# Optimization experiments

Hardware: AMD Instinct MI355X
Metric: run time of the kernel (lower is better)

Reference implementation:

```python
import jax, jax.numpy as jnp
import numpy as np

ROUTING_ITERATIONS = 3

def squash(x, axis=-1):
    # norm_sq/(1+norm_sq) * x/norm, equation 1 of the CapsNet paper
    norm_sq = jnp.sum(x * x, axis=axis, keepdims=True)
    norm = jnp.sqrt(norm_sq)
    return norm_sq / (1.0 + norm_sq) * (x / norm)

def setup_inputs() -> dict:
    key = jax.random.key(0)
    k1, k2 = jax.random.split(key)
    B, IC, IH, OC, OH = 64, 2048, 16, 64, 32
    input_capsules = jax.random.normal(k1, (B, IC, IH), dtype=jnp.float32)
    # scale weight so U entries are O(1) (sum over in_hid=16)
    W = jax.random.normal(k2, (IC, IH, OC, OH), dtype=jnp.float32) * (1.0 / np.sqrt(IH))
    return {"input_capsules": input_capsules, "W": W}

def reference(input_capsules, W):
    # U[b,i,o,j] = sum_h x[b,i,h] * W[i,h,o,j]
    U = jnp.einsum('bih,ihoj->bioj', input_capsules, W)
    b, in_caps, out_caps, out_hid = U.shape
    Blog = jnp.zeros((b, in_caps, out_caps), dtype=U.dtype)

    def body(Blog, _):
        C = jax.nn.softmax(Blog, axis=-1)            # [b,i,o]
        S = jnp.einsum('bio,bioh->boh', C, U)        # [b,o,h]
        V = squash(S, axis=-1)                       # [b,o,h]
        Blog = Blog + jnp.einsum('bioh,boh->bio', U, V)
        return Blog, V

    _, Vs = jax.lax.scan(body, Blog, None, length=ROUTING_ITERATIONS)
    return Vs[-1]
```

## Files before the change

kernel.cpp:

```cpp
#include <hip/hip_runtime.h>
#include <hip/hip_bf16.h>
#include <cstdint>
#include <cstddef>

constexpr int B_SZ = 64, IC = 2048, IH = 16, OC = 64, OH = 32;
constexpr int NN = OC * OH;
constexpr int ICHUNK = 32;
constexpr int NCHUNK = IC / ICHUNK;
constexpr int BTILE = 16;

typedef __attribute__((ext_vector_type(8))) short bf16x8;
typedef __attribute__((ext_vector_type(4))) float f32x4;

constexpr int F_Z = 0;
constexpr int F_W = 64;
constexpr int F_WBUF = 65536;
constexpr int F_T = F_W + 2 * F_WBUF;
constexpr int T_ROW = 80;
constexpr int T_BUF = 16 * T_ROW;
constexpr int F_SMEM = F_T + 2 * T_BUF;

__device__ __forceinline__ unsigned short f2bf(float f) {
    unsigned u = __float_as_uint(f);
    u += 0x7fffu + ((u >> 16) & 1u);
    return (unsigned short)(u >> 16);
}
__device__ __forceinline__ float bf_lo(unsigned u) {
    return __uint_as_float(u << 16);
}
__device__ __forceinline__ float bf_hi(unsigned u) {
    return __uint_as_float(u & 0xffff0000u);
}
__device__ __forceinline__ unsigned pk2f(float a, float b) {
    return (unsigned)f2bf(a) | ((unsigned)f2bf(b) << 16);
}
__device__ __forceinline__ void gload_lds16(const void* g, void* l) {
    __builtin_amdgcn_global_load_lds(
        (const __attribute__((address_space(1))) void*)g,
        (__attribute__((address_space(3))) void*)l, 16, 0, 0);
}

__global__ void prep_wx(const float* __restrict__ W, unsigned short* __restrict__ Wp,
                        const float* __restrict__ x, unsigned short* __restrict__ xs) {
    int i = blockIdx.x;
    int t = threadIdx.x;
    const float* wp = W + (size_t)i * (IH * NN);
    int n0 = t * 4;
    float4 row[16];
#pragma unroll
    for (int h = 0; h < 16; ++h) row[h] = *(const float4*)(wp + h * NN + n0);
    char* dst = (char*)Wp + (size_t)i * 65536;
#pragma unroll
    for (int q = 0; q < 4; ++q) {
        float v[16];
#pragma unroll
        for (int h = 0; h < 16; ++h) v[h] = ((const float*)&row[h])[q];
        uint4 lo, hi;
        lo.x = pk2f(v[0], v[1]);   lo.y = pk2f(v[2], v[3]);
        lo.z = pk2f(v[4], v[5]);   lo.w = pk2f(v[6], v[7]);
        hi.x = pk2f(v[8], v[9]);   hi.y = pk2f(v[10], v[11]);
        hi.z = pk2f(v[12], v[13]); hi.w = pk2f(v[14], v[15]);
        *(uint4*)(dst + (size_t)(n0 + q) * 16) = lo;
        *(uint4*)(dst + 32768 + (size_t)(n0 + q) * 16) = hi;
    }
    if (t < 64) {
        const float* p = x + ((size_t)t * IC + i) * IH;
        unsigned short out[16];
#pragma unroll
        for (int h = 0; h < 16; ++h) out[h] = f2bf(p[h]);
        unsigned short* q = xs + ((size_t)i * 64 + t) * 16;
        *(uint4*)q = *(uint4*)&out[0];
        *(uint4*)(q + 8) = *(uint4*)&out[8];
    }
}

template <bool UNIFORM>
__launch_bounds__(1024, 4)
__global__ void routed_fast(const unsigned short* __restrict__ xs,
                            const unsigned short* __restrict__ Wp,
                            const float* __restrict__ Vin,
                            float* __restrict__ P) {
    extern __shared__ char smem[];
    const int tid = threadIdx.x;
    const int lane = tid & 63;
    const int wv = tid >> 6;
    const int l15 = lane & 15;
    const int g = lane >> 4;

    const int v = blockIdx.x;
    const int bt = (v >> 3) & 3;
    const int chunk = (v & 7) + 8 * (v >> 5);
    const int b0 = bt * BTILE;
    const int i0 = chunk * ICHUNK;

    if (tid < 16) ((unsigned*)(smem + F_Z))[tid] = 0u;

    uint4 vrp[4];
    if constexpr (!UNIFORM) {
#pragma unroll
        for (int o8 = 0; o8 < 4; ++o8) {
            const float* vb =
                Vin + ((size_t)(b0 + l15) * OC + (wv * 4 + o8)) * OH + g * 4;
            f32x4 a = *(const f32x4*)vb;
            f32x4 c = *(const f32x4*)(vb + 16);
            vrp[o8].x = pk2f(a.x, a.y);
            vrp[o8].y = pk2f(a.z, a.w);
            vrp[o8].z = pk2f(c.x, c.y);
            vrp[o8].w = pk2f(c.z, c.w);
        }
    }

    {
        const char* gs = (const char*)Wp + (size_t)i0 * 65536;
#pragma unroll
        for (int r = 0; r < 4; ++r) {
            int seg = r * 16 + wv;
            gload_lds16(gs + seg * 1024 + lane * 16, smem + F_W + seg * 1024);
        }
    }
    bf16x8 xf = {0, 0, 0, 0, 0, 0, 0, 0};
    if (lane < 32)
        xf = *(const bf16x8*)(xs + (size_t)i0 * 1024 + (size_t)(b0 + l15) * 16 + g * 8);
    asm volatile("s_waitcnt vmcnt(0) lgkmcnt(0)" ::: "memory");
    __builtin_amdgcn_s_barrier();

    const f32x4 fzero = {0.f, 0.f, 0.f, 0.f};
    f32x4 sacc[8];
#pragma unroll
    for (int t = 0; t < 8; ++t) sacc[t] = fzero;

    for (int ii = 0; ii < ICHUNK; ++ii) {
        const int cur = ii & 1;
        const char* wb = smem + F_W + cur * F_WBUF;
        const int i = i0 + ii;

        bf16x8 xf_n = {0, 0, 0, 0, 0, 0, 0, 0};
        if (ii + 1 < ICHUNK) {
            const char* gs = (const char*)Wp + (size_t)(i + 1) * 65536;
            char* lb = smem + F_W + (cur ^ 1) * F_WBUF;
#pragma unroll
            for (int r = 0; r < 4; ++r) {
                int seg = r * 16 + wv;
                gload_lds16(gs + seg * 1024 + lane * 16, lb + seg * 1024);
            }
            if (lane < 32)
                xf_n = *(const bf16x8*)(xs + (size_t)(i + 1) * 1024 +
                                        (size_t)(b0 + l15) * 16 + g * 8);
        }

        f32x4 acc[8];
#pragma unroll
        for (int t = 0; t < 8; ++t) {
            int nt = wv * 128 + (t >> 1) * 32 + (t & 1) * 16;
            const char* aptr = (lane < 32)
                ? (wb + g * 32768 + (size_t)(nt + l15) * 16)
                : (smem + F_Z);
            bf16x8 af = *(const bf16x8*)aptr;
            if constexpr (UNIFORM) {
                sacc[t] = __builtin_amdgcn_mfma_f32_16x16x32_bf16(af, xf, sacc[t], 0, 0, 0);
            } else {
                acc[t] = __builtin_amdgcn_mfma_f32_16x16x32_bf16(af, xf, fzero, 0, 0, 0);
            }
        }

        if constexpr (UNIFORM) {
            asm volatile("s_waitcnt vmcnt(0)" ::: "memory");
            __builtin_amdgcn_s_barrier();
        } else {
            float eb[4], s4;
#pragma unroll
            for (int o8 = 0; o8 < 4; ++o8) {
                f32x4 a0 = acc[2 * o8], a1 = acc[2 * o8 + 1];
                uint4 u = vrp[o8];
                float p = a0.x * bf_lo(u.x) + a0.y * bf_hi(u.x) +
                          a0.z * bf_lo(u.y) + a0.w * bf_hi(u.y) +
                          a1.x * bf_lo(u.z) + a1.y * bf_hi(u.z) +
                          a1.z * bf_lo(u.w) + a1.w * bf_hi(u.w);
                p += __shfl_xor(p, 16);
                p += __shfl_xor(p, 32);
                eb[o8] = __expf(p);
            }
            s4 = (eb[0] + eb[1]) + (eb[2] + eb[3]);

            if (lane < 16)
                *(float*)(smem + F_T + cur * T_BUF + l15 * T_ROW + wv * 4) = s4;

            asm volatile("s_waitcnt vmcnt(0) lgkmcnt(0)" ::: "memory");
            __builtin_amdgcn_s_barrier();

            const char* tb = smem + F_T + cur * T_BUF + l15 * T_ROW;
            f32x4 t0 = *(const f32x4*)(tb);
            f32x4 t1 = *(const f32x4*)(tb + 16);
            f32x4 t2 = *(const f32x4*)(tb + 32);
            f32x4 t3 = *(const f32x4*)(tb + 48);
            f32x4 ts = (t0 + t1) + (t2 + t3);
            float denom = (ts.x + ts.y) + (ts.z + ts.w);
            float rd = __builtin_amdgcn_rcpf(denom);
            float c0 = eb[0] * rd, c1 = eb[1] * rd, c2 = eb[2] * rd, c3 = eb[3] * rd;
#pragma unroll
            for (int t = 0; t < 8; ++t) {
                float c = (t < 2) ? c0 : (t < 4) ? c1 : (t < 6) ? c2 : c3;
                sacc[t] += acc[t] * c;
            }
        }
        xf = xf_n;
    }

    const float scale = UNIFORM ? (1.0f / 64.0f) : 1.0f;
#pragma unroll
    for (int t = 0; t < 8; ++t) {
        int n = wv * 128 + (t >> 1) * 32 + (t & 1) * 16 + g * 4;
        float* dst = P + ((size_t)(chunk * 64) + b0 + l15) * NN + n;
        float4 o4;
        o4.x = sacc[t].x * scale; o4.y = sacc[t].y * scale;
        o4.z = sacc[t].z * scale; o4.w = sacc[t].w * scale;
        *(float4*)dst = o4;
    }
}

__global__ void reduce_squash(const float* __restrict__ P, float* __restrict__ dst,
                              int addmode) {
    int pr = blockIdx.x * 2 + (threadIdx.x >> 5);
    int j = threadIdx.x & 31;
    int b = pr >> 6, o = pr & 63;
    const float* p = P + (size_t)b * NN + o * 32 + j;
    float s = 0.f;
#pragma unroll 8
    for (int c = 0; c < NCHUNK; ++c) s += p[(size_t)c * (64 * NN)];
    float nsq = s * s;
#pragma unroll
    for (int d = 16; d >= 1; d >>= 1) nsq += __shfl_xor(nsq, d);
    float nrm = sqrtf(nsq);
    float f = nrm / (1.f + nsq);
    float outv = s * f;
    int idx = pr * 32 + j;
    if (addmode) dst[idx] += outv;
    else dst[idx] = outv;
}

extern "C" void kernel_launch(void* const* d_in, const int* in_sizes, int n_in,
                              void* d_out, int out_size, void* d_ws, size_t ws_size,
                              hipStream_t stream) {
    const float* x = (const float*)d_in[0];
    const float* W = (const float*)d_in[1];
    float* out = (float*)d_out;
    char* ws = (char*)d_ws;
    unsigned short* xs = (unsigned short*)ws;
    float* P = (float*)(ws + ((size_t)4 << 20));
    float* Vsum = (float*)(ws + ((size_t)36 << 20));
    unsigned short* Wp = (unsigned short*)(ws + (((size_t)40) << 20));

    (void)hipFuncSetAttribute(reinterpret_cast<const void*>(&routed_fast<true>),
                              hipFuncAttributeMaxDynamicSharedMemorySize, F_SMEM);
    (void)hipFuncSetAttribute(reinterpret_cast<const void*>(&routed_fast<false>),
                              hipFuncAttributeMaxDynamicSharedMemorySize, F_SMEM);

    prep_wx<<<dim3(2048), dim3(512), 0, stream>>>(W, Wp, x, xs);
    routed_fast<true><<<dim3(256), dim3(1024), F_SMEM, stream>>>(xs, Wp, nullptr, P);
    reduce_squash<<<dim3(2048), dim3(64), 0, stream>>>(P, Vsum, 0);
    routed_fast<false><<<dim3(256), dim3(1024), F_SMEM, stream>>>(xs, Wp, Vsum, P);
    reduce_squash<<<dim3(2048), dim3(64), 0, stream>>>(P, Vsum, 1);
    routed_fast<false><<<dim3(256), dim3(1024), F_SMEM, stream>>>(xs, Wp, Vsum, P);
    reduce_squash<<<dim3(2048), dim3(64), 0, stream>>>(P, out, 0);
}
```

Before: 323.0 us.

## Split uniform pass into dedicated 32x32 MFMA GEMM kernel and streamline routed loop

Replaces the templated uniform-routing path with a separate kernel. It uses 512-thread blocks, splits each chunk's N dimension into quarters, tiles 32 batches per block and runs 32x32x16 bf16 MFMAs with a 32KB double-buffered static LDS tile. This should improve MFMA utilisation and occupancy for the first iteration, which needs no softmax. The routed kernel gains hoisted pointer and offset arithmetic, an unrolled two-buffer loop and a larger zero region so all 64 lanes load x directly. It also uses __syncthreads in place of explicit waitcnt plus barrier. The cost is more blocks and separate code paths to maintain.

```diff
diff --git a/kernel.cpp b/kernel.cpp
--- a/kernel.cpp
+++ b/kernel.cpp
@@ -3,7 +3,7 @@
 #include <cstdint>
 #include <cstddef>
 
-constexpr int B_SZ = 64, IC = 2048, IH = 16, OC = 64, OH = 32;
+constexpr int IC = 2048, IH = 16, OC = 64, OH = 32;
 constexpr int NN = OC * OH;
 constexpr int ICHUNK = 32;
 constexpr int NCHUNK = IC / ICHUNK;
@@ -11,9 +11,10 @@
 
 typedef __attribute__((ext_vector_type(8))) short bf16x8;
 typedef __attribute__((ext_vector_type(4))) float f32x4;
+typedef __attribute__((ext_vector_type(16))) float f32x16;
 
 constexpr int F_Z = 0;
-constexpr int F_W = 64;
+constexpr int F_W = 2048;
 constexpr int F_WBUF = 65536;
 constexpr int F_T = F_W + 2 * F_WBUF;
 constexpr int T_ROW = 80;
@@ -74,9 +75,88 @@
     }
 }
 
-template <bool UNIFORM>
+__launch_bounds__(512, 4)
+__global__ void uniform_gemm(const unsigned short* __restrict__ xs,
+                             const unsigned short* __restrict__ Wp,
+                             float* __restrict__ P) {
+    __shared__ char smem[32768];
+    const int tid = threadIdx.x;
+    const int lane = tid & 63;
+    const int wv = tid >> 6;
+    const int l31 = lane & 31;
+    const int hi = lane >> 5;
+
+    const int v = blockIdx.x;
+    const int chunk = (v & 7) + 8 * (v >> 6);
+    const int sub = (v >> 3) & 7;
+    const int b0 = (sub >> 2) * 32;
+    const int nq = sub & 3;
+    const int i0 = chunk * ICHUNK;
+    const int n0 = nq * 512;
+
+    const char* gW = (const char*)Wp + (size_t)i0 * 65536;
+    int goff[2], loff[2];
+#pragma unroll
+    for (int r = 0; r < 2; ++r) {
+        int m = wv * 2 + r, s = m >> 3, q = m & 7;
+        goff[r] = s * 32768 + n0 * 16 + q * 1024 + lane * 16;
+        loff[r] = s * 8192 + q * 1024;
+    }
+    const int abase = hi * 8192 + wv * 1024 + l31 * 16;
+    const char* gx = (const char*)xs + (size_t)i0 * 2048 + (b0 + l31) * 32 + hi * 16;
+
+#pragma unroll
+    for (int r = 0; r < 2; ++r) gload_lds16(gW + goff[r], smem + loff[r]);
+    bf16x8 xf = *(const bf16x8*)gx;
+    __syncthreads();
+
+    f32x16 sacc[2];
+#pragma unroll
+    for (int t = 0; t < 2; ++t)
+#pragma unroll
+        for (int k = 0; k < 16; ++k) sacc[t][k] = 0.f;
+
+    for (int pp = 0; pp < ICHUNK / 2; ++pp) {
+#pragma unroll
+        for (int cb = 0; cb < 2; ++cb) {
+            const int ii = pp * 2 + cb;
+            bf16x8 xf_n = xf;
+            if (ii + 1 < ICHUNK) {
+                const char* gWn = gW + (size_t)(ii + 1) * 65536;
+                char* nb = smem + (cb ^ 1) * 16384;
+#pragma unroll
+                for (int r = 0; r < 2; ++r) gload_lds16(gWn + goff[r], nb + loff[r]);
+                xf_n = *(const bf16x8*)(gx + (size_t)(ii + 1) * 2048);
+            }
+            const char* ab = smem + cb * 16384 + abase;
+#pragma unroll
+            for (int t = 0; t < 2; ++t) {
+                bf16x8 af = *(const bf16x8*)(ab + t * 512);
+                sacc[t] = __builtin_amdgcn_mfma_f32_32x32x16_bf16(af, xf, sacc[t], 0, 0, 0);
+            }
+            __syncthreads();
+            xf = xf_n;
+        }
+    }
+
+    float* Pb = P + ((size_t)(chunk * 64) + b0 + l31) * NN + n0;
+#pragma unroll
+    for (int t = 0; t < 2; ++t) {
+        int ntl = (wv * 2 + t) * 32;
+#pragma unroll
+        for (int q = 0; q < 4; ++q) {
+            float4 o4;
+            o4.x = sacc[t][4 * q + 0] * (1.0f / 64.0f);
+            o4.y = sacc[t][4 * q + 1] * (1.0f / 64.0f);
+            o4.z = sacc[t][4 * q + 2] * (1.0f / 64.0f);
+            o4.w = sacc[t][4 * q + 3] * (1.0f / 64.0f);
+            *(float4*)(Pb + ntl + 8 * q + 4 * hi) = o4;
+        }
+    }
+}
+
 __launch_bounds__(1024, 4)
-__global__ void routed_fast(const unsigned short* __restrict__ xs,
+__global__ void routed_soft(const unsigned short* __restrict__ xs,
                             const unsigned short* __restrict__ Wp,
                             const float* __restrict__ Vin,
                             float* __restrict__ P) {
@@ -93,81 +173,69 @@
     const int b0 = bt * BTILE;
     const int i0 = chunk * ICHUNK;
 
-    if (tid < 16) ((unsigned*)(smem + F_Z))[tid] = 0u;
+    if (tid < 512) ((unsigned*)(smem + F_Z))[tid] = 0u;
 
     uint4 vrp[4];
-    if constexpr (!UNIFORM) {
-#pragma unroll
-        for (int o8 = 0; o8 < 4; ++o8) {
-            const float* vb =
-                Vin + ((size_t)(b0 + l15) * OC + (wv * 4 + o8)) * OH + g * 4;
-            f32x4 a = *(const f32x4*)vb;
-            f32x4 c = *(const f32x4*)(vb + 16);
-            vrp[o8].x = pk2f(a.x, a.y);
-            vrp[o8].y = pk2f(a.z, a.w);
-            vrp[o8].z = pk2f(c.x, c.y);
-            vrp[o8].w = pk2f(c.z, c.w);
-        }
-    }
-
-    {
-        const char* gs = (const char*)Wp + (size_t)i0 * 65536;
-#pragma unroll
-        for (int r = 0; r < 4; ++r) {
-            int seg = r * 16 + wv;
-            gload_lds16(gs + seg * 1024 + lane * 16, smem + F_W + seg * 1024);
-        }
-    }
-    bf16x8 xf = {0, 0, 0, 0, 0, 0, 0, 0};
-    if (lane < 32)
-        xf = *(const bf16x8*)(xs + (size_t)i0 * 1024 + (size_t)(b0 + l15) * 16 + g * 8);
-    asm volatile("s_waitcnt vmcnt(0) lgkmcnt(0)" ::: "memory");
-    __builtin_amdgcn_s_barrier();
+#pragma unroll
+    for (int o8 = 0; o8 < 4; ++o8) {
+        const float* vb = Vin + ((size_t)(b0 + l15) * OC + (wv * 4 + o8)) * OH + g * 4;
+        f32x4 a = *(const f32x4*)vb;
+        f32x4 c = *(const f32x4*)(vb + 16);
+        vrp[o8].x = pk2f(a.x, a.y); vrp[o8].y = pk2f(a.z, a.w);
+        vrp[o8].z = pk2f(c.x, c.y); vrp[o8].w = pk2f(c.z, c.w);
+    }
+
+    const int a_off = g * 32768 + wv * 2048 + l15 * 16;
+    const char* a_p0 = (lane < 32) ? (smem + F_W + a_off) : (smem + F_Z);
+    const char* a_p1 = (lane < 32) ? (smem + F_W + F_WBUF + a_off) : (smem + F_Z);
+
+    const char* gW = (const char*)Wp + (size_t)i0 * 65536;
+    int goff[4], lds_off[4];
+#pragma unroll
+    for (int r = 0; r < 4; ++r) {
+        int seg = r * 16 + wv;
+        goff[r] = seg * 1024 + lane * 16;
+        lds_off[r] = F_W + seg * 1024;
+    }
+
+    const char* gx = (const char*)xs + (size_t)i0 * 2048 + (b0 + l15) * 32 + (g & 1) * 16;
+
+    char* t_w = smem + F_T + l15 * T_ROW + wv * 4;
+    const char* t_r = smem + F_T + l15 * T_ROW;
+
+#pragma unroll
+    for (int r = 0; r < 4; ++r) gload_lds16(gW + goff[r], smem + lds_off[r]);
+    bf16x8 xf = *(const bf16x8*)gx;
+    __syncthreads();
 
     const f32x4 fzero = {0.f, 0.f, 0.f, 0.f};
     f32x4 sacc[8];
 #pragma unroll
     for (int t = 0; t < 8; ++t) sacc[t] = fzero;
 
-    for (int ii = 0; ii < ICHUNK; ++ii) {
-        const int cur = ii & 1;
-        const char* wb = smem + F_W + cur * F_WBUF;
-        const int i = i0 + ii;
-
-        bf16x8 xf_n = {0, 0, 0, 0, 0, 0, 0, 0};
-        if (ii + 1 < ICHUNK) {
-            const char* gs = (const char*)Wp + (size_t)(i + 1) * 65536;
-            char* lb = smem + F_W + (cur ^ 1) * F_WBUF;
-#pragma unroll
-            for (int r = 0; r < 4; ++r) {
-                int seg = r * 16 + wv;
-                gload_lds16(gs + seg * 1024 + lane * 16, lb + seg * 1024);
-            }
-            if (lane < 32)
-                xf_n = *(const bf16x8*)(xs + (size_t)(i + 1) * 1024 +
-                                        (size_t)(b0 + l15) * 16 + g * 8);
-        }
-
-        f32x4 acc[8];
-#pragma unroll
-        for (int t = 0; t < 8; ++t) {
-            int nt = wv * 128 + (t >> 1) * 32 + (t & 1) * 16;
-            const char* aptr = (lane < 32)
-                ? (wb + g * 32768 + (size_t)(nt + l15) * 16)
-                : (smem + F_Z);
-            bf16x8 af = *(const bf16x8*)aptr;
-            if constexpr (UNIFORM) {
-                sacc[t] = __builtin_amdgcn_mfma_f32_16x16x32_bf16(af, xf, sacc[t], 0, 0, 0);
-            } else {
+    for (int pp = 0; pp < ICHUNK / 2; ++pp) {
+#pragma unroll
+        for (int cb = 0; cb < 2; ++cb) {
+            const int ii = pp * 2 + cb;
+
+            bf16x8 xf_n = xf;
+            if (ii + 1 < ICHUNK) {
+                const char* gWn = gW + (size_t)(ii + 1) * 65536;
+                char* nb = smem + (cb ^ 1) * F_WBUF;
+#pragma unroll
+                for (int r = 0; r < 4; ++r) gload_lds16(gWn + goff[r], nb + lds_off[r]);
+                xf_n = *(const bf16x8*)(gx + (size_t)(ii + 1) * 2048);
+            }
+
+            const char* ap = cb ? a_p1 : a_p0;
+            f32x4 acc[8];
+#pragma unroll
+            for (int t = 0; t < 8; ++t) {
+                bf16x8 af = *(const bf16x8*)(ap + ((t >> 1) * 512 + (t & 1) * 256));
                 acc[t] = __builtin_amdgcn_mfma_f32_16x16x32_bf16(af, xf, fzero, 0, 0, 0);
             }
-        }
-
-        if constexpr (UNIFORM) {
-            asm volatile("s_waitcnt vmcnt(0)" ::: "memory");
-            __builtin_amdgcn_s_barrier();
-        } else {
-            float eb[4], s4;
+
+            float eb[4];
 #pragma unroll
             for (int o8 = 0; o8 < 4; ++o8) {
                 f32x4 a0 = acc[2 * o8], a1 = acc[2 * o8 + 1];
@@ -180,15 +248,12 @@
                 p += __shfl_xor(p, 32);
                 eb[o8] = __expf(p);
             }
-            s4 = (eb[0] + eb[1]) + (eb[2] + eb[3]);
-
-            if (lane < 16)
-                *(float*)(smem + F_T + cur * T_BUF + l15 * T_ROW + wv * 4) = s4;
-
-            asm volatile("s_waitcnt vmcnt(0) lgkmcnt(0)" ::: "memory");
-            __builtin_amdgcn_s_barrier();
-
-            const char* tb = smem + F_T + cur * T_BUF + l15 * T_ROW;
+            float s4 = (eb[0] + eb[1]) + (eb[2] + eb[3]);
+            if (lane < 16) *(float*)(t_w + cb * T_BUF) = s4;
+
+            __syncthreads();
+
+            const char* tb = t_r + cb * T_BUF;
             f32x4 t0 = *(const f32x4*)(tb);
             f32x4 t1 = *(const f32x4*)(tb + 16);
             f32x4 t2 = *(const f32x4*)(tb + 32);
@@ -202,18 +267,16 @@
                 float c = (t < 2) ? c0 : (t < 4) ? c1 : (t < 6) ? c2 : c3;
                 sacc[t] += acc[t] * c;
             }
+            xf = xf_n;
         }
-        xf = xf_n;
-    }
-
-    const float scale = UNIFORM ? (1.0f / 64.0f) : 1.0f;
+    }
+
 #pragma unroll
     for (int t = 0; t < 8; ++t) {
         int n = wv * 128 + (t >> 1) * 32 + (t & 1) * 16 + g * 4;
         float* dst = P + ((size_t)(chunk * 64) + b0 + l15) * NN + n;
         float4 o4;
-        o4.x = sacc[t].x * scale; o4.y = sacc[t].y * scale;
-        o4.z = sacc[t].z * scale; o4.w = sacc[t].w * scale;
+        o4.x = sacc[t].x; o4.y = sacc[t].y; o4.z = sacc[t].z; o4.w = sacc[t].w;
         *(float4*)dst = o4;
     }
 }
@@ -250,16 +313,14 @@
     float* Vsum = (float*)(ws + ((size_t)36 << 20));
     unsigned short* Wp = (unsigned short*)(ws + (((size_t)40) << 20));
 
-    (void)hipFuncSetAttribute(reinterpret_cast<const void*>(&routed_fast<true>),
+    (void)hipFuncSetAttribute(reinterpret_cast<const void*>(&routed_soft),
                               hipFuncAttributeMaxDynamicSharedMemorySize, F_SMEM);
-    (void)hipFuncSetAttribute(reinterpret_cast<const void*>(&routed_fast<false>),
-                              hipFuncAttributeMaxDynamicSharedMemorySize, F_SMEM);
 
     prep_wx<<<dim3(2048), dim3(512), 0, stream>>>(W, Wp, x, xs);
-    routed_fast<true><<<dim3(256), dim3(1024), F_SMEM, stream>>>(xs, Wp, nullptr, P);
+    uniform_gemm<<<dim3(512), dim3(512), 0, stream>>>(xs, Wp, P);
     reduce_squash<<<dim3(2048), dim3(64), 0, stream>>>(P, Vsum, 0);
-    routed_fast<false><<<dim3(256), dim3(1024), F_SMEM, stream>>>(xs, Wp, Vsum, P);
+    routed_soft<<<dim3(256), dim3(1024), F_SMEM, stream>>>(xs, Wp, Vsum, P);
     reduce_squash<<<dim3(2048), dim3(64), 0, stream>>>(P, Vsum, 1);
-    routed_fast<false><<<dim3(256), dim3(1024), F_SMEM, stream>>>(xs, Wp, Vsum, P);
+    routed_soft<<<dim3(256), dim3(1024), F_SMEM, stream>>>(xs, Wp, Vsum, P);
     reduce_squash<<<dim3(2048), dim3(64), 0, stream>>>(P, out, 0);
 }
```

Result: slower. 888.8 us (+175.2%).
